# Kernel optimization log

Measured on AMD Instinct MI355X. Metric: run time of the kernel, lower is better.

The kernel has to match this reference:

```python
import jax, jax.numpy as jnp
import numpy as np

COMMITMENT_COST = 0.25


def setup_inputs() -> dict:
    key = jax.random.key(0)
    k1, k2 = jax.random.split(key)
    inputs = jax.random.normal(k1, (32, 1024, 256), dtype=jnp.float32)
    codebook = jax.random.normal(k2, (8192, 256), dtype=jnp.float32)
    return {"inputs": inputs, "codebook": codebook}


def reference(inputs, codebook):
    input_shape = inputs.shape
    D = codebook.shape[1]
    K = codebook.shape[0]
    flat = inputs.reshape(-1, D)                      # [N, D]
    N = flat.shape[0]

    distances = (
        jnp.sum(flat * flat, axis=1, keepdims=True)
        + jnp.sum(codebook * codebook, axis=1)
        - 2.0 * flat @ codebook.T
    )                                                  # [N, K]
    idx = jnp.argmin(distances, axis=1)               # [N]

    # gather (equivalent to one-hot @ codebook)
    quantized = jnp.take(codebook, idx, axis=0).reshape(input_shape)

    # straight-through estimator
    quantized_st = inputs + jax.lax.stop_gradient(quantized - inputs)

    e_latent_loss = jnp.mean((jax.lax.stop_gradient(quantized_st) - inputs) ** 2)
    q_latent_loss = jnp.mean((quantized - jax.lax.stop_gradient(inputs)) ** 2)
    commitment_loss = COMMITMENT_COST * e_latent_loss
    codebook_loss = q_latent_loss
    vq_loss = commitment_loss + codebook_loss

    # perplexity of codebook usage (avg one-hot probs)
    counts = jnp.zeros((K,), dtype=inputs.dtype).at[idx].add(1.0)
    avg_probs = counts / N
    perplexity = jnp.exp(-jnp.sum(avg_probs * jnp.log(avg_probs + 1e-10)))

    tokens = idx.reshape(input_shape[:-1])
    return quantized_st, tokens, vq_loss, commitment_loss, codebook_loss, perplexity
```

## Files before the change

kernel.cpp:

```cpp
#include <hip/hip_runtime.h>
#include <stdint.h>

typedef unsigned short u16;
typedef unsigned long long u64;

#define N_ROWS 32768
#define DIM 256
#define K_CODES 8192
#define TAU 0.3f

#define A_OFF     0ull
#define B_OFF     16777216ull
#define CN_OFF    20971520ull
#define PART1_OFF 21004288ull
#define PART2_OFF 22052864ull
#define IDX_OFF   22577152ull
#define HIST_OFF  22708224ull
#define CNT_OFF   22740992ull
#define FLAG_OFF  22741008ull
#define LOSS_OFF  22872080ull
#define CBT_OFF   23068672ull
#define GMIN2_OFF 31457280ull

#define OUT_Q 0
#define OUT_T 8388608
#define OUT_S 8421376

#define BM 128
#define BNT 64
#define JSPLIT 4
#define NJC ((K_CODES / JSPLIT) / BNT)
#define RSPLIT 4

#define PACK_INF ((((u64)0xFF800000u) << 32) | 0xFFFFFFFFull)

typedef _Float16 half8 __attribute__((ext_vector_type(8)));
typedef float floatx4 __attribute__((ext_vector_type(4)));

__device__ __forceinline__ void gload_lds16(const void* g, void* l) {
    __builtin_amdgcn_global_load_lds(
        (const __attribute__((address_space(1))) void*)g,
        (__attribute__((address_space(3))) void*)l,
        16, 0, 0);
}
__device__ __forceinline__ void gload_lds4(const void* g, void* l) {
    __builtin_amdgcn_global_load_lds(
        (const __attribute__((address_space(1))) void*)g,
        (__attribute__((address_space(3))) void*)l,
        4, 0, 0);
}

__device__ __forceinline__ unsigned sortable(float v) {
    unsigned u = __float_as_uint(v);
    return (u & 0x80000000u) ? ~u : (u | 0x80000000u);
}
__device__ __forceinline__ float unsortable(unsigned u) {
    return (u & 0x80000000u) ? __uint_as_float(u & 0x7fffffffu) : __uint_as_float(~u);
}
__device__ __forceinline__ u64 shfl64x(u64 v, int m) {
    return ((u64)(unsigned)__shfl_xor((int)(v >> 32), m, 64) << 32) |
           (unsigned)__shfl_xor((int)(v & 0xffffffffu), m, 64);
}
__device__ __forceinline__ u64 u64min(u64 a, u64 b) { return a < b ? a : b; }
__device__ __forceinline__ u64 u64max(u64 a, u64 b) { return a > b ? a : b; }

__global__ void prep(const float* __restrict__ inp, const float* __restrict__ cb,
                     u16* __restrict__ A, u16* __restrict__ B, float* __restrict__ cn) {
    int g = blockIdx.x * 256 + threadIdx.x;
    int row = g >> 5;
    int kc = (g & 31) << 3;
    bool isA = row < N_ROWS;
    const float* src = isA ? inp + (size_t)row * DIM + kc
                           : cb + (size_t)(row - N_ROWS) * DIM + kc;
    u16* dst = isA ? A + (size_t)row * DIM + kc
                   : B + (size_t)(row - N_ROWS) * DIM + kc;
    float4 x0 = *(const float4*)(src);
    float4 x1 = *(const float4*)(src + 4);
    float xs[8] = {x0.x, x0.y, x0.z, x0.w, x1.x, x1.y, x1.z, x1.w};
    half8 hv;
    float s = 0.f;
#pragma unroll
    for (int i = 0; i < 8; ++i) {
        hv[i] = (_Float16)xs[i];
        s = fmaf(xs[i], xs[i], s);
    }
    *(half8*)(dst) = hv;
    if (!isA) {
#pragma unroll
        for (int m = 1; m <= 16; m <<= 1) s += __shfl_xor(s, m, 64);
        if ((g & 31) == 0) cn[row - N_ROWS] = s;
    }
}

__global__ void transpose_cb(const float* __restrict__ cb, float* __restrict__ cbT) {
    __shared__ float tile[64][65];
    const int tid = threadIdx.x;
    const int tj = blockIdx.x * 64;
    const int td = blockIdx.y * 64;
    const int c = (tid & 15) * 4;
    const int r0 = tid >> 4;
#pragma unroll
    for (int p = 0; p < 4; ++p) {
        int r = p * 16 + r0;
        float4 v = *(const float4*)(cb + (size_t)(tj + r) * DIM + td + c);
        tile[r][c] = v.x; tile[r][c + 1] = v.y; tile[r][c + 2] = v.z; tile[r][c + 3] = v.w;
    }
    __syncthreads();
#pragma unroll
    for (int p = 0; p < 4; ++p) {
        int rr = p * 16 + r0;
        float4 w = {tile[c][rr], tile[c + 1][rr], tile[c + 2][rr], tile[c + 3][rr]};
        *(float4*)(cbT + (size_t)(td + rr) * K_CODES + tj + c) = w;
    }
}

#define STAGE_B(BUFP, JCV)                                                    \
    {                                                                         \
        const u16* bsrc_ = B + (size_t)(jBase + (JCV) * BNT) * DIM;           \
        _Pragma("unroll")                                                     \
        for (int r_ = 0; r_ < 4; ++r_) {                                      \
            int idx_ = r_ * 512 + tid;                                        \
            int col_ = idx_ >> 5;                                             \
            int sc_ = idx_ & 31;                                              \
            int csrc_ = (sc_ & 24) | ((sc_ & 7) ^ (col_ & 7));                \
            gload_lds16(bsrc_ + (size_t)col_ * DIM + csrc_ * 8,               \
                        (char*)(BUFP) + idx_ * 16);                           \
        }                                                                     \
        gload_lds4(cn + jBase + (JCV) * BNT + lane,                           \
                   &cnRing[(JCV) & 3][lane]);                                 \
    }

#define TOP2(JT, ACC, CNV)                                                    \
    {                                                                         \
        unsigned jj_ = (unsigned)(jBase + (JT) * BNT + colLoc);               \
        _Pragma("unroll")                                                     \
        for (int mi_ = 0; mi_ < 4; ++mi_) {                                   \
            _Pragma("unroll")                                                 \
            for (int r_ = 0; r_ < 4; ++r_) {                                  \
                int tr_ = mi_ * 4 + r_;                                       \
                float val_ = fmaf(-2.0f, ACC[mi_][r_], (CNV));                \
                float nd2_ = __builtin_amdgcn_fmed3f(d1[tr_], d2[tr_], val_); \
                bool lt_ = val_ < d1[tr_];                                    \
                d1[tr_] = fminf(d1[tr_], val_);                               \
                idxr[tr_] = lt_ ? jj_ : idxr[tr_];                            \
                d2[tr_] = nd2_;                                               \
            }                                                                 \
        }                                                                     \
    }

#define MFMA_TILE(BP, ACC_C)                                                  \
    {                                                                         \
        _Pragma("unroll")                                                     \
        for (int mi_ = 0; mi_ < 4; ++mi_)                                     \
            ACC_C[mi_] = (floatx4){0.f, 0.f, 0.f, 0.f};                       \
        __builtin_amdgcn_s_setprio(1);                                        \
        _Pragma("unroll")                                                     \
        for (int ks_ = 0; ks_ < 8; ++ks_) {                                   \
            const int c_ = ks_ * 4 + quad;                                    \
            const int scw_ = (c_ & 24) | ((c_ & 7) ^ xm);                     \
            half8 bfv_ = *(const half8*)((const char*)(BP) + colLoc * 512 +   \
                                         scw_ * 16);                          \
            _Pragma("unroll")                                                 \
            for (int mi_ = 0; mi_ < 4; ++mi_)                                 \
                ACC_C[mi_] = __builtin_amdgcn_mfma_f32_16x16x32_f16(          \
                    af[mi_][ks_], bfv_, ACC_C[mi_], 0, 0, 0);                 \
        }                                                                     \
        __builtin_amdgcn_s_setprio(0);                                        \
    }

#define TILE(JCV, ACC_C, ACC_P, DO_STAGE, DO_TOP2, WAITN)                     \
    {                                                                         \
        if (DO_STAGE) STAGE_B(bp2, (JCV) + 2);                                \
        if (DO_TOP2) {                                                        \
            float cnv_ = cnRing[((JCV) - 1) & 3][colLoc];                     \
            TOP2((JCV) - 1, ACC_P, cnv_);                                     \
        }                                                                     \
        MFMA_TILE(bp0, ACC_C);                                                \
        if ((WAITN) == 5) asm volatile("s_waitcnt vmcnt(5)" ::: "memory");    \
        else if ((WAITN) == 0) asm volatile("s_waitcnt vmcnt(0)" ::: "memory");\
        __builtin_amdgcn_s_barrier();                                         \
        asm volatile("" ::: "memory");                                        \
        { _Float16* tp_ = bp0; bp0 = bp1; bp1 = bp2; bp2 = tp_; }             \
    }

__launch_bounds__(512, 2)
__global__ void vq_pass1(const u16* __restrict__ A, const u16* __restrict__ B,
                         const float* __restrict__ cn,
                         u64* __restrict__ part1, float* __restrict__ part2) {
    __shared__ __align__(16) _Float16 lsB[3][BNT * DIM];
    __shared__ float cnRing[4][BNT];
    __shared__ u64 t1[8][64];
    __shared__ float t2[8][64];

    const int tid = threadIdx.x;
    const int lane = tid & 63;
    const int w = tid >> 6;
    const int wm = w >> 2;
    const int wn = w & 3;
    const int l15 = lane & 15;
    const int quad = lane >> 4;
    const int xm = l15 & 7;
    const int colLoc = wn * 16 + l15;
    const int rowBase = blockIdx.x * BM;
    const int jBase = blockIdx.y * (K_CODES / JSPLIT);

    _Float16* bp0 = lsB[0];
    _Float16* bp1 = lsB[1];
    _Float16* bp2 = lsB[2];

    half8 af[4][8];
    {
        const u16* aRow = A + (size_t)(rowBase + wm * 64 + l15) * DIM + quad * 8;
#pragma unroll
        for (int mi = 0; mi < 4; ++mi)
#pragma unroll
            for (int ks = 0; ks < 8; ++ks)
                af[mi][ks] = *(const half8*)(aRow + (size_t)mi * 16 * DIM + ks * 32);
    }

    float d1[16], d2[16];
    unsigned idxr[16];
#pragma unroll
    for (int i = 0; i < 16; ++i) {
        d1[i] = __builtin_inff(); d2[i] = __builtin_inff(); idxr[i] = 0xffffffffu;
    }
    floatx4 accA[4], accB[4];

    STAGE_B(bp0, 0);
    STAGE_B(bp1, 1);
    asm volatile("s_waitcnt vmcnt(5)" ::: "memory");
    __builtin_amdgcn_s_barrier();
    asm volatile("" ::: "memory");

#pragma unroll 1
    for (int jc2 = 0; jc2 < NJC - 2; jc2 += 2) {
        TILE(jc2,     accA, accB, true, (jc2 > 0), 5);
        TILE(jc2 + 1, accB, accA, true, true,      5);
    }
    TILE(NJC - 2, accA, accB, false, true, 0);
    TILE(NJC - 1, accB, accA, false, true, -1);
    {
        float cnv_ = cnRing[(NJC - 1) & 3][colLoc];
        TOP2(NJC - 1, accB, cnv_);
    }

    u64 m1[16];
#pragma unroll
    for (int tr = 0; tr < 16; ++tr)
        m1[tr] = ((u64)sortable(d1[tr]) << 32) | idxr[tr];
#pragma unroll
    for (int m = 1; m <= 8; m <<= 1)
#pragma unroll
        for (int tr = 0; tr < 16; ++tr) {
            u64 o1 = shfl64x(m1[tr], m);
            float o2 = __shfl_xor(d2[tr], m, 64);
            u64 n1 = u64min(m1[tr], o1);
            float big = unsortable((unsigned)(u64max(m1[tr], o1) >> 32));
            d2[tr] = fminf(big, fminf(d2[tr], o2));
            m1[tr] = n1;
        }

    if (l15 == 0) {
#pragma unroll
        for (int tr = 0; tr < 16; ++tr) {
            int rl = (tr >> 2) * 16 + quad * 4 + (tr & 3);
            t1[w][rl] = m1[tr];
            t2[w][rl] = d2[tr];
        }
    }
    __syncthreads();
    if (tid < BM) {
        int rg = tid >> 6;
        int rl = tid & 63;
        u64 b1 = t1[rg * 4][rl];
        float b2 = t2[rg * 4][rl];
#pragma unroll
        for (int y = 1; y < 4; ++y) {
            u64 o1 = t1[rg * 4 + y][rl];
            float o2 = t2[rg * 4 + y][rl];
            u64 n1 = u64min(b1, o1);
            float big = unsortable((unsigned)(u64max(b1, o1) >> 32));
            b2 = fminf(big, fminf(b2, o2));
            b1 = n1;
        }
        size_t p = (size_t)(rowBase + tid) * JSPLIT + blockIdx.y;
        part1[p] = b1;
        part2[p] = b2;
    }
}

__global__ void vq_merge(const u64* __restrict__ part1, const float* __restrict__ part2,
                         unsigned* __restrict__ idx32,
                         int* __restrict__ flaglist, int* __restrict__ cnt) {
    int row = blockIdx.x * 256 + threadIdx.x;
    u64 m1 = PACK_INF;
    float f2 = __builtin_inff();
#pragma unroll
    for (int y = 0; y < JSPLIT; ++y) {
        u64 p1 = part1[(size_t)row * JSPLIT + y];
        float p2 = part2[(size_t)row * JSPLIT + y];
        u64 n1 = u64min(m1, p1);
        float big = unsortable((unsigned)(u64max(m1, p1) >> 32));
        f2 = fminf(big, fminf(f2, p2));
        m1 = n1;
    }
    idx32[row] = (unsigned)(m1 & 0xffffffffu);
    float f1 = unsortable((unsigned)(m1 >> 32));
    if (f2 - f1 < TAU) {
        int p = atomicAdd(cnt, 1);
        flaglist[p] = row;
    }
}

__global__ void vq_recompute(const float* __restrict__ inp, const float* __restrict__ cbT,
                             const float* __restrict__ cn, const int* __restrict__ flaglist,
                             const int* __restrict__ cnt, u64* __restrict__ gmin2) {
    __shared__ float xsT[DIM][8];
    __shared__ u64 wred[8][8];
    const int tid = threadIdx.x;
    const int w = tid >> 6, lane = tid & 63;
    const int n = *cnt;
    const int base = blockIdx.x * 8;
    if (base >= n) return;

    {
        int li = base + w;
        int row = flaglist[li < n ? li : (n - 1)];
        float4 a = ((const float4*)(inp + (size_t)row * DIM))[lane];
        int d0 = lane * 4;
        xsT[d0 + 0][w] = a.x; xsT[d0 + 1][w] = a.y;
        xsT[d0 + 2][w] = a.z; xsT[d0 + 3][w] = a.w;
    }
    __syncthreads();

    const int cbase = blockIdx.y * (K_CODES / RSPLIT) + tid * 4;
    float4 acc[8];
#pragma unroll
    for (int r = 0; r < 8; ++r) acc[r] = (float4){0.f, 0.f, 0.f, 0.f};

    float4 cv = *(const float4*)(cbT + cbase);
#pragma unroll 4
    for (int d = 0; d < DIM - 1; ++d) {
        float4 nx = *(const float4*)(cbT + (size_t)(d + 1) * K_CODES + cbase);
        float4 xa = *(const float4*)&xsT[d][0];
        float4 xb = *(const float4*)&xsT[d][4];
        float xv[8] = {xa.x, xa.y, xa.z, xa.w, xb.x, xb.y, xb.z, xb.w};
#pragma unroll
        for (int r = 0; r < 8; ++r) {
            acc[r].x = fmaf(xv[r], cv.x, acc[r].x);
            acc[r].y = fmaf(xv[r], cv.y, acc[r].y);
            acc[r].z = fmaf(xv[r], cv.z, acc[r].z);
            acc[r].w = fmaf(xv[r], cv.w, acc[r].w);
        }
        cv = nx;
    }
    {
        const int d = DIM - 1;
        float4 xa = *(const float4*)&xsT[d][0];
        float4 xb = *(const float4*)&xsT[d][4];
        float xv[8] = {xa.x, xa.y, xa.z, xa.w, xb.x, xb.y, xb.z, xb.w};
#pragma unroll
        for (int r = 0; r < 8; ++r) {
            acc[r].x = fmaf(xv[r], cv.x, acc[r].x);
            acc[r].y = fmaf(xv[r], cv.y, acc[r].y);
            acc[r].z = fmaf(xv[r], cv.z, acc[r].z);
            acc[r].w = fmaf(xv[r], cv.w, acc[r].w);
        }
    }

    u64 best[8];
    float4 cn4 = *(const float4*)(cn + cbase);
#pragma unroll
    for (int r = 0; r < 8; ++r) {
        float d0 = cn4.x - 2.0f * acc[r].x;
        float d1 = cn4.y - 2.0f * acc[r].y;
        float d2 = cn4.z - 2.0f * acc[r].z;
        float d3 = cn4.w - 2.0f * acc[r].w;
        u64 b = ((u64)sortable(d0) << 32) | (unsigned)(cbase + 0);
        b = u64min(b, ((u64)sortable(d1) << 32) | (unsigned)(cbase + 1));
        b = u64min(b, ((u64)sortable(d2) << 32) | (unsigned)(cbase + 2));
        b = u64min(b, ((u64)sortable(d3) << 32) | (unsigned)(cbase + 3));
        best[r] = b;
    }

#pragma unroll
    for (int m = 1; m <= 32; m <<= 1)
#pragma unroll
        for (int r = 0; r < 8; ++r) best[r] = u64min(best[r], shfl64x(best[r], m));
    if (lane < 8) wred[w][lane] = best[lane];
    __syncthreads();
    if (tid < 8 && base + tid < n) {
        u64 b = wred[0][tid];
#pragma unroll
        for (int ww = 1; ww < 8; ++ww) b = u64min(b, wred[ww][tid]);
        atomicMin(&gmin2[flaglist[base + tid]], b);
    }
}

__global__ void vq_writeback(const u64* __restrict__ gmin2, const int* __restrict__ flaglist,
                             const int* __restrict__ cnt, unsigned* __restrict__ idx32) {
    int i = blockIdx.x * 256 + threadIdx.x;
    if (i < *cnt) {
        int row = flaglist[i];
        idx32[row] = (unsigned)(gmin2[row] & 0xffffffffull);
    }
}

__global__ void vq_gather(const float* __restrict__ inp, const float* __restrict__ cb,
                          const unsigned* __restrict__ idx32, float* __restrict__ out,
                          float* __restrict__ losspart, unsigned int* __restrict__ hist) {
    __shared__ float red[4];
    int w = threadIdx.x >> 6, lane = threadIdx.x & 63;
    int i = blockIdx.x * 4 + w;
    unsigned idx = idx32[i];
    float4 c = ((const float4*)(cb + (size_t)idx * DIM))[lane];
    float4 x = ((const float4*)(inp + (size_t)i * DIM))[lane];
    ((float4*)(out + OUT_Q))[(size_t)i * 64 + lane] = c;
    float dx = c.x - x.x, dy = c.y - x.y, dz = c.z - x.z, dw = c.w - x.w;
    float s = dx * dx + dy * dy + dz * dz + dw * dw;
#pragma unroll
    for (int m = 32; m; m >>= 1) s += __shfl_xor(s, m, 64);
    if (lane == 0) {
        out[OUT_T + i] = (float)idx;
        red[w] = s;
        atomicAdd(&hist[idx], 1u);
    }
    __syncthreads();
    if (threadIdx.x == 0)
        losspart[blockIdx.x] = red[0] + red[1] + red[2] + red[3];
}

__global__ void vq_finalize(const unsigned int* __restrict__ hist,
                            const float* __restrict__ losspart, float* __restrict__ out) {
    __shared__ float redp[256], redl[256];
    int tid = threadIdx.x;
    float sp = 0.f, sl = 0.f;
    for (int k = tid; k < K_CODES; k += 256) {
        float p = (float)hist[k] * (1.0f / (float)N_ROWS);
        sp += p * logf(p + 1e-10f);
        sl += losspart[k];
    }
    redp[tid] = sp; redl[tid] = sl;
    __syncthreads();
    for (int st = 128; st; st >>= 1) {
        if (tid < st) { redp[tid] += redp[tid + st]; redl[tid] += redl[tid + st]; }
        __syncthreads();
    }
    if (tid == 0) {
        float perp = expf(-redp[0]);
        float e = redl[0] / 8388608.0f;
        out[OUT_S + 0] = 1.25f * e;
        out[OUT_S + 1] = 0.25f * e;
        out[OUT_S + 2] = e;
        out[OUT_S + 3] = perp;
    }
}

extern "C" void kernel_launch(void* const* d_in, const int* in_sizes, int n_in,
                              void* d_out, int out_size, void* d_ws, size_t ws_size,
                              hipStream_t stream) {
    const float* inp = (const float*)d_in[0];
    const float* cb = (const float*)d_in[1];
    float* out = (float*)d_out;
    char* ws = (char*)d_ws;
    u16* A = (u16*)(ws + A_OFF);
    u16* B = (u16*)(ws + B_OFF);
    float* cn = (float*)(ws + CN_OFF);
    u64* part1 = (u64*)(ws + PART1_OFF);
    float* part2 = (float*)(ws + PART2_OFF);
    unsigned* idx32 = (unsigned*)(ws + IDX_OFF);
    unsigned int* hist = (unsigned int*)(ws + HIST_OFF);
    int* cnt = (int*)(ws + CNT_OFF);
    int* flaglist = (int*)(ws + FLAG_OFF);
    float* losspart = (float*)(ws + LOSS_OFF);
    float* cbT = (float*)(ws + CBT_OFF);
    u64* gmin2 = (u64*)(ws + GMIN2_OFF);

    hipMemsetAsync(hist, 0, K_CODES * 4 + 16, stream);
    hipMemsetAsync(gmin2, 0xFF, N_ROWS * 8, stream);

    prep<<<5120, 256, 0, stream>>>(inp, cb, A, B, cn);
    transpose_cb<<<dim3(K_CODES / 64, DIM / 64), 256, 0, stream>>>(cb, cbT);
    vq_pass1<<<dim3(N_ROWS / BM, JSPLIT), 512, 0, stream>>>(A, B, cn, part1, part2);
    vq_merge<<<N_ROWS / 256, 256, 0, stream>>>(part1, part2, idx32, flaglist, cnt);
    vq_recompute<<<dim3(N_ROWS / 8, RSPLIT), 512, 0, stream>>>(inp, cbT, cn, flaglist, cnt, gmin2);
    vq_writeback<<<N_ROWS / 256, 256, 0, stream>>>(gmin2, flaglist, cnt, idx32);
    vq_gather<<<N_ROWS / 4, 256, 0, stream>>>(inp, cb, idx32, out, losspart, hist);
    vq_finalize<<<1, 256, 0, stream>>>(hist, losspart, out);
}
```

Baseline: 418.7 us.

## Deepen B-tile pipeline to 4 buffers with split-phase LDS prefetch

Restructures the pass-1 main loop into two half-phases per tile. B fragments for the next half are read from LDS into registers while the current MFMAs run, and the global-to-LDS staging and top-2 update are split across the halves. LDS buffering grows from 3 to 4 tiles, giving a prefetch distance of three tiles. The aim is to hide LDS read latency and spread VMEM issue. The cost is more LDS, extra barriers per tile, more registers for the fragment sets, and complex vmcnt bookkeeping that could be wrong at the loop tail.

```diff
diff --git a/kernel.cpp b/kernel.cpp
--- a/kernel.cpp
+++ b/kernel.cpp
@@ -31,6 +31,7 @@
 #define JSPLIT 4
 #define NJC ((K_CODES / JSPLIT) / BNT)
 #define RSPLIT 4
+#define TB (BNT * DIM * 2)
 
 #define PACK_INF ((((u64)0xFF800000u) << 32) | 0xFFFFFFFFull)
 
@@ -114,11 +115,19 @@
     }
 }
 
-#define STAGE_B(BUFP, JCV)                                                    \
+
+#define DSR1(DST, BASE, KS)                                                   \
+    {                                                                         \
+        const int c_ = (KS) * 4 + quad;                                       \
+        const int scw_ = (c_ & 24) | ((c_ & 7) ^ xm);                         \
+        DST = *(const half8*)((BASE) + colLoc * 512 + scw_ * 16);             \
+    }
+
+#define STAGE_PART(BUFP, JCV, R0, NR)                                         \
     {                                                                         \
         const u16* bsrc_ = B + (size_t)(jBase + (JCV) * BNT) * DIM;           \
         _Pragma("unroll")                                                     \
-        for (int r_ = 0; r_ < 4; ++r_) {                                      \
+        for (int r_ = (R0); r_ < (R0) + (NR); ++r_) {                         \
             int idx_ = r_ * 512 + tid;                                        \
             int col_ = idx_ >> 5;                                             \
             int sc_ = idx_ & 31;                                              \
@@ -126,19 +135,17 @@
             gload_lds16(bsrc_ + (size_t)col_ * DIM + csrc_ * 8,               \
                         (char*)(BUFP) + idx_ * 16);                           \
         }                                                                     \
-        gload_lds4(cn + jBase + (JCV) * BNT + lane,                           \
-                   &cnRing[(JCV) & 3][lane]);                                 \
-    }
-
-#define TOP2(JT, ACC, CNV)                                                    \
+    }
+
+#define TOP2H(JT, ACC, MI0)                                                   \
     {                                                                         \
         unsigned jj_ = (unsigned)(jBase + (JT) * BNT + colLoc);               \
         _Pragma("unroll")                                                     \
-        for (int mi_ = 0; mi_ < 4; ++mi_) {                                   \
+        for (int mi_ = (MI0); mi_ < (MI0) + 2; ++mi_) {                       \
             _Pragma("unroll")                                                 \
             for (int r_ = 0; r_ < 4; ++r_) {                                  \
                 int tr_ = mi_ * 4 + r_;                                       \
-                float val_ = fmaf(-2.0f, ACC[mi_][r_], (CNV));                \
+                float val_ = fmaf(-2.0f, ACC[mi_][r_], cnv);                  \
                 float nd2_ = __builtin_amdgcn_fmed3f(d1[tr_], d2[tr_], val_); \
                 bool lt_ = val_ < d1[tr_];                                    \
                 d1[tr_] = fminf(d1[tr_], val_);                               \
@@ -148,47 +155,54 @@
         }                                                                     \
     }
 
-#define MFMA_TILE(BP, ACC_C)                                                  \
+#define PHASE(JCV, H, ACC_C, ACC_P, BC_, BN_, RB_, DO_RD, DO_STAGE, DO_TOP2)  \
     {                                                                         \
-        _Pragma("unroll")                                                     \
-        for (int mi_ = 0; mi_ < 4; ++mi_)                                     \
-            ACC_C[mi_] = (floatx4){0.f, 0.f, 0.f, 0.f};                       \
+        __builtin_amdgcn_s_barrier();                                         \
+        asm volatile("s_waitcnt lgkmcnt(0)" ::: "memory");                    \
+        __builtin_amdgcn_sched_barrier(0);                                    \
+        if ((H) == 0 && (DO_TOP2)) cnv = cnRing[((JCV) - 1) & 7][colLoc];     \
+        if ((H) == 0) {                                                       \
+            _Pragma("unroll")                                                 \
+            for (int mi_ = 0; mi_ < 4; ++mi_)                                 \
+                ACC_C[mi_] = (floatx4){0.f, 0.f, 0.f, 0.f};                   \
+        }                                                                     \
         __builtin_amdgcn_s_setprio(1);                                        \
         _Pragma("unroll")                                                     \
-        for (int ks_ = 0; ks_ < 8; ++ks_) {                                   \
-            const int c_ = ks_ * 4 + quad;                                    \
-            const int scw_ = (c_ & 24) | ((c_ & 7) ^ xm);                     \
-            half8 bfv_ = *(const half8*)((const char*)(BP) + colLoc * 512 +   \
-                                         scw_ * 16);                          \
+        for (int k2_ = 0; k2_ < 4; ++k2_) {                                   \
+            if (DO_RD) DSR1(BN_[k2_], RB_, ((H) ^ 1) * 4 + k2_);              \
             _Pragma("unroll")                                                 \
             for (int mi_ = 0; mi_ < 4; ++mi_)                                 \
                 ACC_C[mi_] = __builtin_amdgcn_mfma_f32_16x16x32_f16(          \
-                    af[mi_][ks_], bfv_, ACC_C[mi_], 0, 0, 0);                 \
+                    af[mi_][(H) * 4 + k2_], BC_[k2_], ACC_C[mi_], 0, 0, 0);   \
         }                                                                     \
         __builtin_amdgcn_s_setprio(0);                                        \
-    }
-
-#define TILE(JCV, ACC_C, ACC_P, DO_STAGE, DO_TOP2, WAITN)                     \
+        if (DO_STAGE) {                                                       \
+            STAGE_PART(bS, (JCV) + 3, (H) * 2, 2);                            \
+            if ((H) == 0)                                                     \
+                gload_lds4(cn + jBase + ((JCV) + 3) * BNT + lane,             \
+                           &cnRing[((JCV) + 3) & 7][lane]);                   \
+        }                                                                     \
+        if (DO_TOP2) TOP2H((JCV) - 1, ACC_P, (H) * 2);                        \
+    }
+
+#define TILE(JCV, ACC_C, ACC_P, DO_STAGE, DO_TOP2, DO_RD1, WAITN)             \
     {                                                                         \
-        if (DO_STAGE) STAGE_B(bp2, (JCV) + 2);                                \
-        if (DO_TOP2) {                                                        \
-            float cnv_ = cnRing[((JCV) - 1) & 3][colLoc];                     \
-            TOP2((JCV) - 1, ACC_P, cnv_);                                     \
-        }                                                                     \
-        MFMA_TILE(bp0, ACC_C);                                                \
+        const char* bR_ = (const char*)lsB + ((JCV) & 3) * TB;                \
+        const char* bR1_ = (const char*)lsB + (((JCV) + 1) & 3) * TB;         \
+        char* bS = (char*)lsB + (((JCV) + 3) & 3) * TB;                       \
+        PHASE(JCV, 0, ACC_C, ACC_P, bfvE, bfvO, bR_, 1, DO_STAGE, DO_TOP2);   \
+        PHASE(JCV, 1, ACC_C, ACC_P, bfvO, bfvE, bR1_, DO_RD1,                 \
+              DO_STAGE, DO_TOP2);                                             \
         if ((WAITN) == 5) asm volatile("s_waitcnt vmcnt(5)" ::: "memory");    \
-        else if ((WAITN) == 0) asm volatile("s_waitcnt vmcnt(0)" ::: "memory");\
-        __builtin_amdgcn_s_barrier();                                         \
-        asm volatile("" ::: "memory");                                        \
-        { _Float16* tp_ = bp0; bp0 = bp1; bp1 = bp2; bp2 = tp_; }             \
+        else if ((WAITN) == 0) asm volatile("s_waitcnt vmcnt(0)" ::: "memory"); \
     }
 
 __launch_bounds__(512, 2)
 __global__ void vq_pass1(const u16* __restrict__ A, const u16* __restrict__ B,
                          const float* __restrict__ cn,
                          u64* __restrict__ part1, float* __restrict__ part2) {
-    __shared__ __align__(16) _Float16 lsB[3][BNT * DIM];
-    __shared__ float cnRing[4][BNT];
+    __shared__ __align__(16) _Float16 lsB[4][BNT * DIM];
+    __shared__ float cnRing[8][BNT];
     __shared__ u64 t1[8][64];
     __shared__ float t2[8][64];
 
@@ -204,10 +218,6 @@
     const int rowBase = blockIdx.x * BM;
     const int jBase = blockIdx.y * (K_CODES / JSPLIT);
 
-    _Float16* bp0 = lsB[0];
-    _Float16* bp1 = lsB[1];
-    _Float16* bp2 = lsB[2];
-
     half8 af[4][8];
     {
         const u16* aRow = A + (size_t)(rowBase + wm * 64 + l15) * DIM + quad * 8;
@@ -218,6 +228,13 @@
                 af[mi][ks] = *(const half8*)(aRow + (size_t)mi * 16 * DIM + ks * 32);
     }
 
+    STAGE_PART((char*)lsB, 0, 0, 4);
+    gload_lds4(cn + jBase + 0 * BNT + lane, &cnRing[0][lane]);
+    STAGE_PART((char*)lsB + TB, 1, 0, 4);
+    gload_lds4(cn + jBase + 1 * BNT + lane, &cnRing[1][lane]);
+    STAGE_PART((char*)lsB + 2 * TB, 2, 0, 4);
+    gload_lds4(cn + jBase + 2 * BNT + lane, &cnRing[2][lane]);
+
     float d1[16], d2[16];
     unsigned idxr[16];
 #pragma unroll
@@ -225,24 +242,25 @@
         d1[i] = __builtin_inff(); d2[i] = __builtin_inff(); idxr[i] = 0xffffffffu;
     }
     floatx4 accA[4], accB[4];
-
-    STAGE_B(bp0, 0);
-    STAGE_B(bp1, 1);
+    half8 bfvE[4], bfvO[4];
+    float cnv = 0.f;
+
     asm volatile("s_waitcnt vmcnt(5)" ::: "memory");
     __builtin_amdgcn_s_barrier();
     asm volatile("" ::: "memory");
+#pragma unroll
+    for (int k2 = 0; k2 < 4; ++k2) DSR1(bfvE[k2], (const char*)lsB, k2);
 
 #pragma unroll 1
-    for (int jc2 = 0; jc2 < NJC - 2; jc2 += 2) {
-        TILE(jc2,     accA, accB, true, (jc2 > 0), 5);
-        TILE(jc2 + 1, accB, accA, true, true,      5);
-    }
-    TILE(NJC - 2, accA, accB, false, true, 0);
-    TILE(NJC - 1, accB, accA, false, true, -1);
-    {
-        float cnv_ = cnRing[(NJC - 1) & 3][colLoc];
-        TOP2(NJC - 1, accB, cnv_);
-    }
+    for (int jc2 = 0; jc2 < NJC; jc2 += 2) {
+        TILE(jc2, accA, accB, (jc2 + 3 < NJC), (jc2 > 0), 1,
+             (jc2 <= 28 ? 5 : -1));
+        TILE(jc2 + 1, accB, accA, (jc2 + 4 < NJC), 1, (jc2 + 1 < NJC - 1),
+             (jc2 + 1 <= 28 ? 5 : (jc2 + 1 == 29 ? 0 : -1)));
+    }
+    cnv = cnRing[(NJC - 1) & 7][colLoc];
+    TOP2H(NJC - 1, accB, 0);
+    TOP2H(NJC - 1, accB, 2);
 
     u64 m1[16];
 #pragma unroll
```

New measurement: 615.4 us. 1.47x slower.
